# Kernel tuning notes

Hardware: AMD Instinct MI355X
Metric: run time of the kernel (lower is better)

## Reference

```python
import jax, jax.numpy as jnp
import numpy as np

B, S, D, H = 8, 1024, 1024, 16
HD = D // H  # head dim = 64


def setup_inputs() -> dict:
    key = jax.random.key(0)
    ks = jax.random.split(key, 8)
    return {
        "hidden_states": jax.random.normal(ks[0], (B, S, D), dtype=jnp.float32),
        "attention_mask": jnp.zeros((B, 1, 1, S), dtype=jnp.float32),
        "Wq": jax.random.normal(ks[1], (D, D), dtype=jnp.float32) * (1.0 / np.sqrt(D)),
        "bq": jax.random.normal(ks[2], (D,), dtype=jnp.float32) * 0.02,
        "Wk": jax.random.normal(ks[3], (D, D), dtype=jnp.float32) * (1.0 / np.sqrt(D)),
        "bk": jax.random.normal(ks[4], (D,), dtype=jnp.float32) * 0.02,
        "Wv": jax.random.normal(ks[5], (D, D), dtype=jnp.float32) * (1.0 / np.sqrt(D)),
        "bv": jax.random.normal(ks[6], (D,), dtype=jnp.float32) * 0.02,
    }


def _split_heads(x):
    # [B,S,D] -> [B,H,S,HD]
    return x.reshape(B, S, H, HD).transpose(0, 2, 1, 3)


def reference(hidden_states, attention_mask, Wq, bq, Wk, bk, Wv, bv):
    q = _split_heads(hidden_states @ Wq + bq)
    k = _split_heads(hidden_states @ Wk + bk)
    v = _split_heads(hidden_states @ Wv + bv)
    # [B,H,S,S]
    scores = jnp.einsum("bhqd,bhkd->bhqk", q, k) / jnp.sqrt(jnp.float32(HD))
    scores = scores + attention_mask
    probs = jax.nn.softmax(scores, axis=-1)  # dropout p=0.0 (eval)
    ctx = jnp.einsum("bhqk,bhkd->bhqd", probs, v)
    # [B,H,S,HD] -> [B,S,D]
    return ctx.transpose(0, 2, 1, 3).reshape(B, S, D)
```

## Files before the change

### kernel.cpp

```cpp
#include <hip/hip_runtime.h>
#include <stdint.h>

#define BB 8
#define SS 1024
#define DD 1024
#define HH 16
#define HDIM 64

typedef __bf16 bf16x8 __attribute__((ext_vector_type(8)));
typedef float f32x4 __attribute__((ext_vector_type(4)));

__device__ __forceinline__ unsigned short f2bf(float f) {
    union { float f; unsigned u; } v; v.f = f;
    unsigned r = v.u + 0x7fff + ((v.u >> 16) & 1);
    return (unsigned short)(r >> 16);
}

__device__ __forceinline__ float exp2fast(float x) {
#if __has_builtin(__builtin_amdgcn_exp2f)
    return __builtin_amdgcn_exp2f(x);
#else
    return __expf(x * 0.69314718f);
#endif
}

__device__ __forceinline__ void async16(void* lds, const void* g) {
    __builtin_amdgcn_global_load_lds(
        (const __attribute__((address_space(1))) unsigned int*)g,
        (__attribute__((address_space(3))) unsigned int*)lds, 16, 0, 0);
}

__global__ __launch_bounds__(256) void prep(
    const float* __restrict__ x, unsigned short* __restrict__ xf,
    const float* __restrict__ w0, const float* __restrict__ w1,
    const float* __restrict__ w2,
    unsigned short* __restrict__ f0, unsigned short* __restrict__ f1,
    unsigned short* __restrict__ f2)
{
    __shared__ unsigned short tile[64 * 76];
    int bid = blockIdx.x;
    int tid = threadIdx.x;
    if (bid < 2048) {
        int mt = bid >> 4, kt = bid & 15;
        const float* src = x + (size_t)(mt * 64) * DD + kt * 64;
        #pragma unroll
        for (int i = 0; i < 4; ++i) {
            int f = tid + i * 256;
            int r = f >> 4, c4 = f & 15;
            float4 v = *reinterpret_cast<const float4*>(src + r * DD + c4 * 4);
            ushort4 o;
            o.x = f2bf(v.x); o.y = f2bf(v.y); o.z = f2bf(v.z); o.w = f2bf(v.w);
            *reinterpret_cast<ushort4*>(&tile[r * 76 + c4 * 4]) = o;
        }
        __syncthreads();
        #pragma unroll
        for (int i = 0; i < 2; ++i) {
            int s = tid + i * 256;
            int frag = s >> 6, l = s & 63;
            int m_l = (frag & 3) * 16 + (l & 15);
            int k_l = (frag >> 2) * 32 + ((l >> 4) & 3) * 8;
            uint4 v = *reinterpret_cast<const uint4*>(&tile[m_l * 76 + k_l]);
            int fm = mt * 4 + (frag & 3);
            int fk = kt * 2 + (frag >> 2);
            *reinterpret_cast<uint4*>(xf + (size_t)((fm * 32 + fk) * 64 + l) * 8) = v;
        }
        return;
    }
    int idx = bid - 2048;
    int z = idx >> 8, rem = idx & 255;
    const float* w = (z == 0) ? w0 : (z == 1) ? w1 : w2;
    unsigned short* wf = (z == 0) ? f0 : (z == 1) ? f1 : f2;
    int kt = rem & 15, nt = rem >> 4;
    const float* src = w + (size_t)(kt * 64) * DD + nt * 64;
    #pragma unroll
    for (int i = 0; i < 4; ++i) {
        int f = tid + i * 256;
        int r = f >> 4, c4 = f & 15;
        float4 v = *reinterpret_cast<const float4*>(src + r * DD + c4 * 4);
        ushort4 o;
        o.x = f2bf(v.x); o.y = f2bf(v.y); o.z = f2bf(v.z); o.w = f2bf(v.w);
        *reinterpret_cast<ushort4*>(&tile[r * 76 + c4 * 4]) = o;
    }
    __syncthreads();
    #pragma unroll
    for (int i = 0; i < 2; ++i) {
        int s = tid + i * 256;
        int frag = s >> 6, l = s & 63;
        int n_l = (frag & 3) * 16 + (l & 15);
        int k_l = (frag >> 2) * 32 + ((l >> 4) & 3) * 8;
        unsigned short tmp[8];
        #pragma unroll
        for (int j = 0; j < 8; ++j) tmp[j] = tile[(k_l + j) * 76 + n_l];
        int fn = nt * 4 + (frag & 3);
        int fk = kt * 2 + (frag >> 2);
        *reinterpret_cast<uint4*>(wf + (size_t)((fn * 32 + fk) * 64 + l) * 8) =
            *reinterpret_cast<const uint4*>(tmp);
    }
}

__global__ __launch_bounds__(256, 3) void gemm_qkv(
    const unsigned short* __restrict__ xf,
    const unsigned short* __restrict__ wf0, const unsigned short* __restrict__ wf1,
    const unsigned short* __restrict__ wf2,
    const float* __restrict__ b0, const float* __restrict__ b1, const float* __restrict__ b2,
    unsigned short* __restrict__ qo, unsigned short* __restrict__ ko,
    unsigned short* __restrict__ vto)
{
    int bid = blockIdx.x;
    int xcd = bid & 7, g = bid >> 3;
    int strip = xcd * 3 + (g % 3);
    int mt = g / 3;
    int nt = strip & 7, z = strip >> 3;

    const unsigned short* wf; const float* bias; unsigned short* out;
    if (z == 0)      { wf = wf0; bias = b0; out = qo; }
    else if (z == 1) { wf = wf1; bias = b1; out = ko; }
    else             { wf = wf2; bias = b2; out = vto; }

    __shared__ unsigned short stg[4][64 * 76];

    int tid = threadIdx.x;
    int wave = tid >> 6, lane = tid & 63, lq = lane >> 4, lm = lane & 15;
    int wr = wave >> 1, wc = wave & 1;

    const unsigned short* aB = xf + (size_t)((mt * 8 + wr * 4) * 32) * 512 + lane * 8;
    const unsigned short* bB = wf + (size_t)((nt * 8 + wc * 4) * 32) * 512 + lane * 8;

    f32x4 acc[4][4] = {};
    bf16x8 a0[4], a1[4], bb0[4], bb1[4];

#define LDFRAGS(AB, BB, T)                                                     \
    {                                                                          \
        _Pragma("unroll") for (int i_ = 0; i_ < 4; ++i_)                       \
            AB[i_] = *reinterpret_cast<const bf16x8*>(aB + (i_ * 32 + (T)) * 512); \
        _Pragma("unroll") for (int j_ = 0; j_ < 4; ++j_)                       \
            BB[j_] = *reinterpret_cast<const bf16x8*>(bB + (j_ * 32 + (T)) * 512); \
    }
#define MFMAS(AB, BB)                                                          \
    {                                                                          \
        _Pragma("unroll") for (int i_ = 0; i_ < 4; ++i_)                       \
            _Pragma("unroll") for (int j_ = 0; j_ < 4; ++j_)                   \
                acc[i_][j_] = __builtin_amdgcn_mfma_f32_16x16x32_bf16(         \
                    AB[i_], BB[j_], acc[i_][j_], 0, 0, 0);                     \
    }

    LDFRAGS(a0, bb0, 0);
    for (int tt = 0; tt < 16; ++tt) {
        int t = tt * 2;
        LDFRAGS(a1, bb1, t + 1);
        MFMAS(a0, bb0);
        LDFRAGS(a0, bb0, t + 2);
        MFMAS(a1, bb1);
    }
#undef LDFRAGS
#undef MFMAS

    int m0 = mt * 128;
    int col0 = nt * 128 + wc * 64;
    if (z == 2) {
        #pragma unroll
        for (int j = 0; j < 4; ++j) {
            int col = col0 + j * 16 + lm;
            float bsv = bias[col];
            int h = col >> 6, hd = col & 63;
            #pragma unroll
            for (int i = 0; i < 4; ++i) {
                int m = m0 + wr * 64 + i * 16 + lq * 4;
                int b_ = m >> 10, sr = m & 1023;
                union { float f; unsigned u; } p0, p1, p2, p3;
                p0.f = acc[i][j][0] + bsv; p1.f = acc[i][j][1] + bsv;
                p2.f = acc[i][j][2] + bsv; p3.f = acc[i][j][3] + bsv;
                uint2 pk;
                pk.x = __builtin_amdgcn_perm(p1.u + 0x8000u, p0.u + 0x8000u, 0x07060302u);
                pk.y = __builtin_amdgcn_perm(p3.u + 0x8000u, p2.u + 0x8000u, 0x07060302u);
                *reinterpret_cast<uint2*>(out + (((b_ * HH + h) * HDIM + hd) << 10) + sr) = pk;
            }
        }
    } else {
        unsigned short* S = stg[wave];
        #pragma unroll
        for (int j = 0; j < 4; ++j) {
            float bsv = bias[col0 + j * 16 + lm];
            #pragma unroll
            for (int i = 0; i < 4; ++i) {
                #pragma unroll
                for (int r = 0; r < 4; ++r) {
                    union { float f; unsigned u; } cv; cv.f = acc[i][j][r] + bsv;
                    S[(i * 16 + lq * 4 + r) * 76 + j * 16 + lm] =
                        (unsigned short)((cv.u + 0x8000u) >> 16);
                }
            }
        }
        int h = col0 >> 6;
        int mrow = m0 + wr * 64;
        int b_ = mrow >> 10, sr0 = mrow & 1023;
        unsigned short* ob = out + ((size_t)((b_ * HH + h) << 10) + sr0) * HDIM;
        #pragma unroll
        for (int u = 0; u < 8; ++u) {
            int s = lane + u * 64;
            int row = s >> 3, c8 = s & 7;
            uint4 v = *reinterpret_cast<const uint4*>(&S[row * 76 + c8 * 8]);
            *reinterpret_cast<uint4*>(ob + row * HDIM + c8 * 8) = v;
        }
    }
}

__global__ __launch_bounds__(256, 4) void attention(
    const unsigned short* __restrict__ q,
    const unsigned short* __restrict__ k,
    const unsigned short* __restrict__ vt,
    const float* __restrict__ mask,
    float* __restrict__ out)
{
    __shared__ unsigned short Ks[2][64 * 64];
    __shared__ unsigned short Vs[2][64 * 64];
    __shared__ unsigned short Ps[4][16 * 64];

    int blk = blockIdx.x;
    int xcd = blk & 7, j = blk >> 3;
    int bh = (xcd << 4) + (j >> 3);
    int qt = j & 7;
    int b = bh >> 4, h = bh & 15;

    int tid = threadIdx.x;
    int wave = tid >> 6, lane = tid & 63, lq = lane >> 4, lm = lane & 15;

    const unsigned short* qp = q + (size_t)bh * SS * HDIM;
    const unsigned short* kp = k + (size_t)bh * SS * HDIM;
    const unsigned short* vp = vt + (size_t)bh * HDIM * SS;
    const float* maskb = mask + b * SS;

    int qbase = qt * 128 + wave * 16 + lm;
    bf16x8 qa00 = *reinterpret_cast<const bf16x8*>(qp + qbase * HDIM + lq * 8);
    bf16x8 qa01 = *reinterpret_cast<const bf16x8*>(qp + qbase * HDIM + 32 + lq * 8);
    bf16x8 qa10 = *reinterpret_cast<const bf16x8*>(qp + (qbase + 64) * HDIM + lq * 8);
    bf16x8 qa11 = *reinterpret_cast<const bf16x8*>(qp + (qbase + 64) * HDIM + 32 + lq * 8);

    float lsum0 = 0.f, lsum1 = 0.f;
    f32x4 o0[4] = {}, o1[4] = {};

    int row0 = tid >> 3, sg = tid & 7;
    int cg = (sg - row0) & 7;
    const unsigned short* gk = kp + row0 * 64 + cg * 8;
    const unsigned short* gv = vp + row0 * SS + cg * 8;

    int sl0 = ((lq + lm) & 7) * 8;
    int sl1 = ((lq + lm + 4) & 7) * 8;
    unsigned short* Pw = Ps[wave];
    int pwbase = lm * 64 + (lq & 1) * 4;
    int prd0 = lm * 64 + sl0;
    int prd1 = lm * 64 + sl1;

    async16(&Ks[0][tid * 8], gk);  async16(&Ks[0][(tid + 256) * 8], gk + 32 * 64);
    async16(&Vs[0][tid * 8], gv);  async16(&Vs[0][(tid + 256) * 8], gv + 32 * SS);
    gk += 64 * 64; gv += 64;

    for (int t = 0; t < 16; ++t) {
        int p = t & 1;
        __syncthreads();
        int kb0 = t * 64;

        float4 mk[4];
        #pragma unroll
        for (int nb = 0; nb < 4; ++nb) {
            mk[nb] = *reinterpret_cast<const float4*>(maskb + kb0 + nb * 16 + lq * 4);
            #pragma unroll
            for (int r = 0; r < 4; ++r)
                reinterpret_cast<float*>(&mk[nb])[r] *= 1.44269504f;
        }
        if (t < 15) {
            async16(&Ks[p ^ 1][tid * 8], gk);  async16(&Ks[p ^ 1][(tid + 256) * 8], gk + 32 * 64);
            async16(&Vs[p ^ 1][tid * 8], gv);  async16(&Vs[p ^ 1][(tid + 256) * 8], gv + 32 * SS);
            gk += 64 * 64; gv += 64;
        }

        f32x4 c0[4], c1[4];
        #pragma unroll
        for (int nb = 0; nb < 4; ++nb) {
            bf16x8 kf0 = *reinterpret_cast<const bf16x8*>(&Ks[p][(nb * 16 + lm) * 64 + sl0]);
            bf16x8 kf1 = *reinterpret_cast<const bf16x8*>(&Ks[p][(nb * 16 + lm) * 64 + sl1]);
            f32x4 z = {};
            z = __builtin_amdgcn_mfma_f32_16x16x32_bf16(kf0, qa00, z, 0, 0, 0);
            z = __builtin_amdgcn_mfma_f32_16x16x32_bf16(kf1, qa01, z, 0, 0, 0);
            c0[nb] = z;
            f32x4 w = {};
            w = __builtin_amdgcn_mfma_f32_16x16x32_bf16(kf0, qa10, w, 0, 0, 0);
            w = __builtin_amdgcn_mfma_f32_16x16x32_bf16(kf1, qa11, w, 0, 0, 0);
            c1[nb] = w;
        }

        #pragma unroll
        for (int nb = 0; nb < 4; ++nb) {
            unsigned u[4];
            #pragma unroll
            for (int r = 0; r < 4; ++r) {
                float e = exp2fast(fmaf(c0[nb][r], 0.18033688f,
                                        reinterpret_cast<const float*>(&mk[nb])[r]));
                union { float f; unsigned v; } cv; cv.f = e;
                u[r] = cv.v;
                union { unsigned v; float f; } tr; tr.v = cv.v & 0xffff0000u;
                lsum0 += tr.f;
            }
            uint2 pk;
            pk.x = __builtin_amdgcn_perm(u[1], u[0], 0x07060302u);
            pk.y = __builtin_amdgcn_perm(u[3], u[2], 0x07060302u);
            *reinterpret_cast<uint2*>(
                &Pw[pwbase + (((nb * 2 + (lq >> 1)) + lm) & 7) * 8]) = pk;
        }
        bf16x8 pa00 = *reinterpret_cast<const bf16x8*>(&Pw[prd0]);
        bf16x8 pa01 = *reinterpret_cast<const bf16x8*>(&Pw[prd1]);

        #pragma unroll
        for (int nb = 0; nb < 4; ++nb) {
            unsigned u[4];
            #pragma unroll
            for (int r = 0; r < 4; ++r) {
                float e = exp2fast(fmaf(c1[nb][r], 0.18033688f,
                                        reinterpret_cast<const float*>(&mk[nb])[r]));
                union { float f; unsigned v; } cv; cv.f = e;
                u[r] = cv.v;
                union { unsigned v; float f; } tr; tr.v = cv.v & 0xffff0000u;
                lsum1 += tr.f;
            }
            uint2 pk;
            pk.x = __builtin_amdgcn_perm(u[1], u[0], 0x07060302u);
            pk.y = __builtin_amdgcn_perm(u[3], u[2], 0x07060302u);
            *reinterpret_cast<uint2*>(
                &Pw[pwbase + (((nb * 2 + (lq >> 1)) + lm) & 7) * 8]) = pk;
        }
        bf16x8 pa10 = *reinterpret_cast<const bf16x8*>(&Pw[prd0]);
        bf16x8 pa11 = *reinterpret_cast<const bf16x8*>(&Pw[prd1]);

        #pragma unroll
        for (int nb2 = 0; nb2 < 4; ++nb2) {
            bf16x8 vf0 = *reinterpret_cast<const bf16x8*>(&Vs[p][(nb2 * 16 + lm) * 64 + sl0]);
            o0[nb2] = __builtin_amdgcn_mfma_f32_16x16x32_bf16(pa00, vf0, o0[nb2], 0, 0, 0);
            o1[nb2] = __builtin_amdgcn_mfma_f32_16x16x32_bf16(pa10, vf0, o1[nb2], 0, 0, 0);
            bf16x8 vf1 = *reinterpret_cast<const bf16x8*>(&Vs[p][(nb2 * 16 + lm) * 64 + sl1]);
            o0[nb2] = __builtin_amdgcn_mfma_f32_16x16x32_bf16(pa01, vf1, o0[nb2], 0, 0, 0);
            o1[nb2] = __builtin_amdgcn_mfma_f32_16x16x32_bf16(pa11, vf1, o1[nb2], 0, 0, 0);
        }
    }

    lsum0 += __shfl_xor(lsum0, 16, 64);
    lsum0 += __shfl_xor(lsum0, 32, 64);
    lsum1 += __shfl_xor(lsum1, 16, 64);
    lsum1 += __shfl_xor(lsum1, 32, 64);
    float linv0[4], linv1[4];
    #pragma unroll
    for (int r = 0; r < 4; ++r) {
        linv0[r] = 1.0f / __shfl(lsum0, lq * 4 + r, 64);
        linv1[r] = 1.0f / __shfl(lsum1, lq * 4 + r, 64);
    }

    int srb = qt * 128 + wave * 16;
    #pragma unroll
    for (int nb2 = 0; nb2 < 4; ++nb2) {
        #pragma unroll
        for (int r = 0; r < 4; ++r) {
            int sr = srb + lq * 4 + r;
            out[((size_t)(b * SS + sr)) * DD + h * HDIM + nb2 * 16 + lm] =
                o0[nb2][r] * linv0[r];
            out[((size_t)(b * SS + sr + 64)) * DD + h * HDIM + nb2 * 16 + lm] =
                o1[nb2][r] * linv1[r];
        }
    }
}

extern "C" void kernel_launch(void* const* d_in, const int* in_sizes, int n_in,
                              void* d_out, int out_size, void* d_ws, size_t ws_size,
                              hipStream_t stream) {
    const float* hs   = (const float*)d_in[0];
    const float* mask = (const float*)d_in[1];
    const float* Wq   = (const float*)d_in[2];
    const float* bq   = (const float*)d_in[3];
    const float* Wk   = (const float*)d_in[4];
    const float* bk   = (const float*)d_in[5];
    const float* Wv   = (const float*)d_in[6];
    const float* bv   = (const float*)d_in[7];
    float* out = (float*)d_out;

    char* ws = (char*)d_ws;
    unsigned short* XF  = (unsigned short*)(ws);
    unsigned short* WF0 = (unsigned short*)(ws + 16777216);
    unsigned short* WF1 = (unsigned short*)(ws + 18874368);
    unsigned short* WF2 = (unsigned short*)(ws + 20971520);
    unsigned short* qw  = (unsigned short*)(ws + 23068672);
    unsigned short* kw  = (unsigned short*)(ws + 39845888);
    unsigned short* vtw = (unsigned short*)(ws + 56623104);

    prep<<<2816, 256, 0, stream>>>(hs, XF, Wq, Wk, Wv, WF0, WF1, WF2);
    gemm_qkv<<<1536, 256, 0, stream>>>(XF, WF0, WF1, WF2,
                                       bq, bk, bv, qw, kw, vtw);
    attention<<<1024, 256, 0, stream>>>(qw, kw, vtw, mask, out);
}
```

Baseline: 217.2 us.

## Stage QKV GEMM tiles through swizzled LDS with async double-buffered loads

The QKV projection GEMM used to read pre-fragmented bf16 operands straight from global memory into registers. It now stages 128x64 A and B tiles into LDS using async global-to-LDS loads, double-buffered, with an XOR-style rotation swizzle to avoid bank conflicts. Each tile is now shared by all four waves instead of being loaded redundantly per wave. The prep kernel is simplified accordingly: X becomes a plain row-major bf16 conversion and W is stored transposed row-major. LDS use grows to 64KB per block and the occupancy hint drops from 3 to 2 blocks, which may limit latency hiding.

Measured after the change: 216.8 us. About the same (-0.2%).

```diff
diff --git a/kernel.cpp b/kernel.cpp
--- a/kernel.cpp
+++ b/kernel.cpp
@@ -31,42 +31,28 @@
 }
 
 __global__ __launch_bounds__(256) void prep(
-    const float* __restrict__ x, unsigned short* __restrict__ xf,
+    const float* __restrict__ x, unsigned short* __restrict__ xb,
     const float* __restrict__ w0, const float* __restrict__ w1,
     const float* __restrict__ w2,
     unsigned short* __restrict__ f0, unsigned short* __restrict__ f1,
     unsigned short* __restrict__ f2)
 {
-    __shared__ unsigned short tile[64 * 76];
     int bid = blockIdx.x;
     int tid = threadIdx.x;
-    if (bid < 2048) {
-        int mt = bid >> 4, kt = bid & 15;
-        const float* src = x + (size_t)(mt * 64) * DD + kt * 64;
-        #pragma unroll
-        for (int i = 0; i < 4; ++i) {
-            int f = tid + i * 256;
-            int r = f >> 4, c4 = f & 15;
-            float4 v = *reinterpret_cast<const float4*>(src + r * DD + c4 * 4);
-            ushort4 o;
-            o.x = f2bf(v.x); o.y = f2bf(v.y); o.z = f2bf(v.z); o.w = f2bf(v.w);
-            *reinterpret_cast<ushort4*>(&tile[r * 76 + c4 * 4]) = o;
-        }
-        __syncthreads();
-        #pragma unroll
-        for (int i = 0; i < 2; ++i) {
-            int s = tid + i * 256;
-            int frag = s >> 6, l = s & 63;
-            int m_l = (frag & 3) * 16 + (l & 15);
-            int k_l = (frag >> 2) * 32 + ((l >> 4) & 3) * 8;
-            uint4 v = *reinterpret_cast<const uint4*>(&tile[m_l * 76 + k_l]);
-            int fm = mt * 4 + (frag & 3);
-            int fk = kt * 2 + (frag >> 2);
-            *reinterpret_cast<uint4*>(xf + (size_t)((fm * 32 + fk) * 64 + l) * 8) = v;
-        }
+    if (bid < 4096) {
+        size_t base = ((size_t)bid << 11) + tid * 8;
+        float4 v0 = *reinterpret_cast<const float4*>(x + base);
+        float4 v1 = *reinterpret_cast<const float4*>(x + base + 4);
+        union { unsigned short u16[8]; uint4 v; } o;
+        o.u16[0] = f2bf(v0.x); o.u16[1] = f2bf(v0.y);
+        o.u16[2] = f2bf(v0.z); o.u16[3] = f2bf(v0.w);
+        o.u16[4] = f2bf(v1.x); o.u16[5] = f2bf(v1.y);
+        o.u16[6] = f2bf(v1.z); o.u16[7] = f2bf(v1.w);
+        *reinterpret_cast<uint4*>(xb + base) = o.v;
         return;
     }
-    int idx = bid - 2048;
+    __shared__ unsigned short tile[64 * 76];
+    int idx = bid - 4096;
     int z = idx >> 8, rem = idx & 255;
     const float* w = (z == 0) ? w0 : (z == 1) ? w1 : w2;
     unsigned short* wf = (z == 0) ? f0 : (z == 1) ? f1 : f2;
@@ -85,75 +71,117 @@
     #pragma unroll
     for (int i = 0; i < 2; ++i) {
         int s = tid + i * 256;
-        int frag = s >> 6, l = s & 63;
-        int n_l = (frag & 3) * 16 + (l & 15);
-        int k_l = (frag >> 2) * 32 + ((l >> 4) & 3) * 8;
+        int r = s >> 3, c8 = s & 7;
         unsigned short tmp[8];
         #pragma unroll
-        for (int j = 0; j < 8; ++j) tmp[j] = tile[(k_l + j) * 76 + n_l];
-        int fn = nt * 4 + (frag & 3);
-        int fk = kt * 2 + (frag >> 2);
-        *reinterpret_cast<uint4*>(wf + (size_t)((fn * 32 + fk) * 64 + l) * 8) =
+        for (int j = 0; j < 8; ++j) tmp[j] = tile[(c8 * 8 + j) * 76 + r];
+        *reinterpret_cast<uint4*>(wf + (size_t)(nt * 64 + r) * DD + kt * 64 + c8 * 8) =
             *reinterpret_cast<const uint4*>(tmp);
     }
 }
 
-__global__ __launch_bounds__(256, 3) void gemm_qkv(
-    const unsigned short* __restrict__ xf,
-    const unsigned short* __restrict__ wf0, const unsigned short* __restrict__ wf1,
-    const unsigned short* __restrict__ wf2,
+__global__ __launch_bounds__(256, 2) void gemm_qkv(
+    const unsigned short* __restrict__ xb,
+    const unsigned short* __restrict__ wt0, const unsigned short* __restrict__ wt1,
+    const unsigned short* __restrict__ wt2,
     const float* __restrict__ b0, const float* __restrict__ b1, const float* __restrict__ b2,
     unsigned short* __restrict__ qo, unsigned short* __restrict__ ko,
     unsigned short* __restrict__ vto)
 {
+    __shared__ unsigned short SH[32768];
+
     int bid = blockIdx.x;
     int xcd = bid & 7, g = bid >> 3;
     int strip = xcd * 3 + (g % 3);
     int mt = g / 3;
     int nt = strip & 7, z = strip >> 3;
 
-    const unsigned short* wf; const float* bias; unsigned short* out;
-    if (z == 0)      { wf = wf0; bias = b0; out = qo; }
-    else if (z == 1) { wf = wf1; bias = b1; out = ko; }
-    else             { wf = wf2; bias = b2; out = vto; }
-
-    __shared__ unsigned short stg[4][64 * 76];
+    const unsigned short* wt; const float* bias; unsigned short* out;
+    if (z == 0)      { wt = wt0; bias = b0; out = qo; }
+    else if (z == 1) { wt = wt1; bias = b1; out = ko; }
+    else             { wt = wt2; bias = b2; out = vto; }
 
     int tid = threadIdx.x;
     int wave = tid >> 6, lane = tid & 63, lq = lane >> 4, lm = lane & 15;
     int wr = wave >> 1, wc = wave & 1;
 
-    const unsigned short* aB = xf + (size_t)((mt * 8 + wr * 4) * 32) * 512 + lane * 8;
-    const unsigned short* bB = wf + (size_t)((nt * 8 + wc * 4) * 32) * 512 + lane * 8;
+    const unsigned short* sA[4]; const unsigned short* sB[4];
+    int dOff[4];
+    #pragma unroll
+    for (int s = 0; s < 4; ++s) {
+        int o = tid + s * 256;
+        int rw = o >> 3, cs = o & 7;
+        int cl = (cs - rw) & 7;
+        dOff[s] = o * 8;
+        sA[s] = xb + (size_t)(mt * 128 + rw) * DD + cl * 8;
+        sB[s] = wt + (size_t)(nt * 128 + rw) * DD + cl * 8;
+    }
+
+#define STAGE(P, KT)                                                          \
+    {                                                                         \
+        _Pragma("unroll") for (int s_ = 0; s_ < 4; ++s_)                      \
+            async16(&SH[(P) * 8192 + dOff[s_]], sA[s_] + (KT) * 64);          \
+        _Pragma("unroll") for (int s_ = 0; s_ < 4; ++s_)                      \
+            async16(&SH[16384 + (P) * 8192 + dOff[s_]], sB[s_] + (KT) * 64);  \
+    }
+
+    int rA[4][2], rB[4][2];
+    #pragma unroll
+    for (int i = 0; i < 4; ++i) {
+        int rwA = wr * 64 + i * 16 + lm;
+        int rwB = wc * 64 + i * 16 + lm;
+        #pragma unroll
+        for (int ks = 0; ks < 2; ++ks) {
+            rA[i][ks] = rwA * 64 + (((ks * 4 + lq) + rwA) & 7) * 8;
+            rB[i][ks] = rwB * 64 + (((ks * 4 + lq) + rwB) & 7) * 8;
+        }
+    }
 
     f32x4 acc[4][4] = {};
-    bf16x8 a0[4], a1[4], bb0[4], bb1[4];
-
-#define LDFRAGS(AB, BB, T)                                                     \
-    {                                                                          \
-        _Pragma("unroll") for (int i_ = 0; i_ < 4; ++i_)                       \
-            AB[i_] = *reinterpret_cast<const bf16x8*>(aB + (i_ * 32 + (T)) * 512); \
-        _Pragma("unroll") for (int j_ = 0; j_ < 4; ++j_)                       \
-            BB[j_] = *reinterpret_cast<const bf16x8*>(bB + (j_ * 32 + (T)) * 512); \
-    }
-#define MFMAS(AB, BB)                                                          \
-    {                                                                          \
-        _Pragma("unroll") for (int i_ = 0; i_ < 4; ++i_)                       \
-            _Pragma("unroll") for (int j_ = 0; j_ < 4; ++j_)                   \
-                acc[i_][j_] = __builtin_amdgcn_mfma_f32_16x16x32_bf16(         \
-                    AB[i_], BB[j_], acc[i_][j_], 0, 0, 0);                     \
-    }
-
-    LDFRAGS(a0, bb0, 0);
-    for (int tt = 0; tt < 16; ++tt) {
-        int t = tt * 2;
-        LDFRAGS(a1, bb1, t + 1);
-        MFMAS(a0, bb0);
-        LDFRAGS(a0, bb0, t + 2);
-        MFMAS(a1, bb1);
-    }
-#undef LDFRAGS
-#undef MFMAS
+
+#define COMPUTE(P)                                                            \
+    {                                                                         \
+        const unsigned short* Abuf = &SH[(P) * 8192];                         \
+        const unsigned short* Bbuf = &SH[16384 + (P) * 8192];                 \
+        _Pragma("unroll") for (int ks_ = 0; ks_ < 2; ++ks_) {                 \
+            bf16x8 af[4], bf[4];                                              \
+            _Pragma("unroll") for (int i_ = 0; i_ < 4; ++i_)                  \
+                af[i_] = *reinterpret_cast<const bf16x8*>(Abuf + rA[i_][ks_]);\
+            _Pragma("unroll") for (int j_ = 0; j_ < 4; ++j_)                  \
+                bf[j_] = *reinterpret_cast<const bf16x8*>(Bbuf + rB[j_][ks_]);\
+            _Pragma("unroll") for (int i_ = 0; i_ < 4; ++i_)                  \
+                _Pragma("unroll") for (int j_ = 0; j_ < 4; ++j_)              \
+                    acc[i_][j_] = __builtin_amdgcn_mfma_f32_16x16x32_bf16(    \
+                        af[i_], bf[j_], acc[i_][j_], 0, 0, 0);                \
+        }                                                                     \
+    }
+
+    STAGE(0, 0);
+    STAGE(1, 1);
+
+    for (int kt = 0; kt < 14; ++kt) {
+        int p = kt & 1;
+        asm volatile("s_waitcnt vmcnt(8)" ::: "memory");
+        __builtin_amdgcn_s_barrier();
+        __builtin_amdgcn_sched_barrier(0);
+        COMPUTE(p);
+        asm volatile("s_waitcnt lgkmcnt(0)" ::: "memory");
+        __builtin_amdgcn_sched_barrier(0);
+        __builtin_amdgcn_s_barrier();
+        STAGE(p, kt + 2);
+    }
+    asm volatile("s_waitcnt vmcnt(8)" ::: "memory");
+    __builtin_amdgcn_s_barrier();
+    __builtin_amdgcn_sched_barrier(0);
+    COMPUTE(0);
+    asm volatile("s_waitcnt vmcnt(0)" ::: "memory");
+    __builtin_amdgcn_s_barrier();
+    __builtin_amdgcn_sched_barrier(0);
+    COMPUTE(1);
+#undef STAGE
+#undef COMPUTE
+
+    __syncthreads();
 
     int m0 = mt * 128;
     int col0 = nt * 128 + wc * 64;
@@ -177,7 +205,7 @@
             }
         }
     } else {
-        unsigned short* S = stg[wave];
+        unsigned short* S = SH + wave * 4864;
         #pragma unroll
         for (int j = 0; j < 4; ++j) {
             float bsv = bias[col0 + j * 16 + lm];
@@ -381,16 +409,16 @@
     float* out = (float*)d_out;
 
     char* ws = (char*)d_ws;
-    unsigned short* XF  = (unsigned short*)(ws);
-    unsigned short* WF0 = (unsigned short*)(ws + 16777216);
-    unsigned short* WF1 = (unsigned short*)(ws + 18874368);
-    unsigned short* WF2 = (unsigned short*)(ws + 20971520);
+    unsigned short* XB  = (unsigned short*)(ws);
+    unsigned short* WT0 = (unsigned short*)(ws + 16777216);
+    unsigned short* WT1 = (unsigned short*)(ws + 18874368);
+    unsigned short* WT2 = (unsigned short*)(ws + 20971520);
     unsigned short* qw  = (unsigned short*)(ws + 23068672);
     unsigned short* kw  = (unsigned short*)(ws + 39845888);
     unsigned short* vtw = (unsigned short*)(ws + 56623104);
 
-    prep<<<2816, 256, 0, stream>>>(hs, XF, Wq, Wk, Wv, WF0, WF1, WF2);
-    gemm_qkv<<<1536, 256, 0, stream>>>(XF, WF0, WF1, WF2,
+    prep<<<4864, 256, 0, stream>>>(hs, XB, Wq, Wk, Wv, WT0, WT1, WT2);
+    gemm_qkv<<<1536, 256, 0, stream>>>(XB, WT0, WT1, WT2,
                                        bq, bk, bv, qw, kw, vtw);
     attention<<<1024, 256, 0, stream>>>(qw, kw, vtw, mask, out);
 }
```
